# Kernel tuning notes

Measured on AMD Instinct MI355X. Metric: run time of the kernel, lower is better.

Reference implementation:

```python
import jax, jax.numpy as jnp
import numpy as np

DIM = 768      # embedding dim
NH = 12        # num heads
HD = DIM // NH # head dim = 64
WS = 7         # window size
BASE = 100.0   # rope base
TAU = 0.01     # cosine attention temperature


def _rope_tables(Wn):
    # 2D RoPE: first half of head_dim rotates with row index, second half with col index.
    quarter = HD // 4
    inv = BASE ** (-2.0 * jnp.arange(quarter, dtype=jnp.float32) / (HD // 2))  # [HD/4]
    yy, xx = jnp.meshgrid(jnp.arange(Wn, dtype=jnp.float32),
                          jnp.arange(Wn, dtype=jnp.float32), indexing='ij')
    ang = jnp.concatenate([yy.reshape(-1, 1) * inv, xx.reshape(-1, 1) * inv], axis=-1)  # [W^2, HD/2]
    return jnp.sin(ang), jnp.cos(ang)


def _apply_rope(t, sin, cos):
    # t: [Bw, L, nH, HD]; rotate-half within each spatial-axis block
    h = HD // 2
    t1, t2 = t[..., :h], t[..., h:]
    s = sin[None, :, None, :]
    c = cos[None, :, None, :]
    return jnp.concatenate([t1 * c - t2 * s, t1 * s + t2 * c], axis=-1)


def setup_inputs() -> dict:
    key = jax.random.key(0)
    k1, k2, k3 = jax.random.split(key, 3)
    B, H, W_img = 2, 224, 224
    x = jax.random.normal(k1, (B, H * W_img, DIM), jnp.float32)
    qkv_w = jax.random.normal(k2, (3 * DIM, DIM), jnp.float32) * 0.02
    proj_w = jax.random.normal(k3, (DIM, DIM), jnp.float32) * 0.02
    return {"x": x, "qkv_w": qkv_w, "proj_w": proj_w, "H": H, "W_img": W_img, "shift": 1}


def reference(x, qkv_w, proj_w, H, W_img, shift):
    B, N, D = x.shape
    Wn = WS
    x2d = x.reshape(B, H, W_img, D)
    ss = Wn // 2 if shift else 0
    if shift:
        x2d = jnp.roll(x2d, (-ss, -ss), axis=(1, 2))
    pad_b = (-H) % Wn
    pad_r = (-W_img) % Wn
    if pad_b or pad_r:
        x2d = jnp.pad(x2d, ((0, 0), (0, pad_b), (0, pad_r), (0, 0)))
    Hp, Wp = H + pad_b, W_img + pad_r
    # window partition: [B, Hp, Wp, D] -> [B*nW, W^2, D]
    xw = x2d.reshape(B, Hp // Wn, Wn, Wp // Wn, Wn, D).transpose(0, 1, 3, 2, 4, 5).reshape(-1, Wn * Wn, D)
    Bw, L = xw.shape[0], Wn * Wn
    qkv = xw @ qkv_w.T                       # [Bw, L, 3D]
    q, k, v = jnp.split(qkv, 3, axis=-1)
    q = q.reshape(Bw, L, NH, HD)
    k = k.reshape(Bw, L, NH, HD)
    v = v.reshape(Bw, L, NH, HD)
    sin, cos = _rope_tables(Wn)
    q = _apply_rope(q, sin, cos)
    k = _apply_rope(k, sin, cos)
    # cosine attention: L2-normalize q,k then scale by 1/tau
    q = q / jnp.clip(jnp.linalg.norm(q, axis=-1, keepdims=True), 1e-12)
    k = k / jnp.clip(jnp.linalg.norm(k, axis=-1, keepdims=True), 1e-12)
    q = q.transpose(0, 2, 1, 3)  # [Bw, nH, L, HD]
    k = k.transpose(0, 2, 1, 3)
    v = v.transpose(0, 2, 1, 3)
    attn = jax.nn.softmax(jnp.einsum('bhqd,bhkd->bhqk', q, k) / TAU, axis=-1)
    out = jnp.einsum('bhqk,bhkd->bhqd', attn, v)
    out = out.transpose(0, 2, 1, 3).reshape(Bw, L, D)
    # window reverse
    out = out.reshape(B, Hp // Wn, Wp // Wn, Wn, Wn, D).transpose(0, 1, 3, 2, 4, 5).reshape(B, Hp, Wp, D)
    out = out[:, :H, :W_img, :]
    if shift:
        out = jnp.roll(out, (ss, ss), axis=(1, 2))
    return out.reshape(B, N, D) @ proj_w.T
```

## Files before the change

### kernel.cpp

```cpp
#include <hip/hip_runtime.h>
#include <cstdint>
#include <cstddef>

typedef __bf16 bf16x8 __attribute__((ext_vector_type(8)));
typedef float  f32x4  __attribute__((ext_vector_type(4)));

typedef __attribute__((address_space(1))) void v_as1;
typedef __attribute__((address_space(3))) void v_as3;

#define NTOK 100352
#define DIMC 768
#define NHEAD 12
#define IMG 224
#define WN 7
#define WL 49

__device__ __forceinline__ unsigned short f2bf(float f) {
    uint32_t u = __float_as_uint(f);
    uint32_t r = (u + 0x7FFFu + ((u >> 16) & 1u)) >> 16;
    return (unsigned short)r;
}
__device__ __forceinline__ float bf2f(unsigned short u) {
    return __uint_as_float(((uint32_t)u) << 16);
}

__device__ __forceinline__ void async_cp16(const void* g, void* l) {
    __builtin_amdgcn_global_load_lds((v_as1*)g, (v_as3*)l, 16, 0, 0);
}

__global__ __launch_bounds__(256) void hilo_kernel(const float* __restrict__ in,
        unsigned short* __restrict__ hi, unsigned short* __restrict__ lo,
        int n4, int has_lo) {
    int idx = blockIdx.x * 256 + threadIdx.x;
    int stride = gridDim.x * 256;
    for (int i = idx; i < n4; i += stride) {
        float4 v = reinterpret_cast<const float4*>(in)[i];
        ushort4 h;
        h.x = f2bf(v.x); h.y = f2bf(v.y); h.z = f2bf(v.z); h.w = f2bf(v.w);
        reinterpret_cast<ushort4*>(hi)[i] = h;
        if (has_lo) {
            ushort4 l;
            l.x = f2bf(v.x - bf2f(h.x));
            l.y = f2bf(v.y - bf2f(h.y));
            l.z = f2bf(v.z - bf2f(h.z));
            l.w = f2bf(v.w - bf2f(h.w));
            reinterpret_cast<ushort4*>(lo)[i] = l;
        }
    }
}

#define BM 128
#define BN 128
#define BK 32
template <int TRIPLE>
__global__ __launch_bounds__(256) void gemm_bt(
    const unsigned short* __restrict__ Ahi, const unsigned short* __restrict__ Alo,
    const unsigned short* __restrict__ Bhi, const unsigned short* __restrict__ Blo,
    float* __restrict__ Cf, unsigned short* __restrict__ Cb,
    int M, int N, int K)
{
    __shared__ unsigned short lAh[BM * BK];
    __shared__ unsigned short lBh[BN * BK];
    __shared__ unsigned short lAl[BM * BK];
    __shared__ unsigned short lBl[BN * BK];

    const int tid  = threadIdx.x;
    const int wave = tid >> 6;
    const int lane = tid & 63;

    const int nTiles = N / BN;
    const int bm = blockIdx.x / nTiles;
    const int bn = blockIdx.x % nTiles;
    const int m0 = bm * BM, n0 = bn * BN;

    const int wm = (wave & 1) * 64;
    const int wn = (wave >> 1) * 64;

    f32x4 acc[4][4];
#pragma unroll
    for (int i = 0; i < 4; i++)
#pragma unroll
        for (int j = 0; j < 4; j++) acc[i][j] = (f32x4){0.f, 0.f, 0.f, 0.f};

    const int c0 = tid, c1 = tid + 256;
    const int ar0 = c0 >> 2, ac0 = (c0 & 3) * 8;
    const int ar1 = c1 >> 2, ac1 = (c1 & 3) * 8;
    const size_t off0 = (size_t)(wave * 64) * 8;
    const size_t off1 = (size_t)(256 + wave * 64) * 8;

    const int lquad = lane >> 4;
    const int l16   = lane & 15;

    const unsigned short* AhB = Ahi + (size_t)m0 * K;
    const unsigned short* BhB = Bhi + (size_t)n0 * K;
    const unsigned short* AlB = TRIPLE ? Alo + (size_t)m0 * K : nullptr;
    const unsigned short* BlB = TRIPLE ? Blo + (size_t)n0 * K : nullptr;

    for (int kk = 0; kk < K; kk += BK) {
        async_cp16(AhB + (size_t)ar0 * K + kk + ac0, &lAh[off0]);
        async_cp16(AhB + (size_t)ar1 * K + kk + ac1, &lAh[off1]);
        async_cp16(BhB + (size_t)ar0 * K + kk + ac0, &lBh[off0]);
        async_cp16(BhB + (size_t)ar1 * K + kk + ac1, &lBh[off1]);
        if (TRIPLE) {
            async_cp16(AlB + (size_t)ar0 * K + kk + ac0, &lAl[off0]);
            async_cp16(AlB + (size_t)ar1 * K + kk + ac1, &lAl[off1]);
            async_cp16(BlB + (size_t)ar0 * K + kk + ac0, &lBl[off0]);
            async_cp16(BlB + (size_t)ar1 * K + kk + ac1, &lBl[off1]);
        }
        __syncthreads();
        bf16x8 ah[4], bh[4];
#pragma unroll
        for (int i = 0; i < 4; i++)
            ah[i] = *reinterpret_cast<const bf16x8*>(&lAh[(size_t)(wm + i * 16 + l16) * BK + lquad * 8]);
#pragma unroll
        for (int j = 0; j < 4; j++)
            bh[j] = *reinterpret_cast<const bf16x8*>(&lBh[(size_t)(wn + j * 16 + l16) * BK + lquad * 8]);
#pragma unroll
        for (int i = 0; i < 4; i++)
#pragma unroll
            for (int j = 0; j < 4; j++)
                acc[i][j] = __builtin_amdgcn_mfma_f32_16x16x32_bf16(ah[i], bh[j], acc[i][j], 0, 0, 0);
        if (TRIPLE) {
            bf16x8 al[4], bl[4];
#pragma unroll
            for (int i = 0; i < 4; i++)
                al[i] = *reinterpret_cast<const bf16x8*>(&lAl[(size_t)(wm + i * 16 + l16) * BK + lquad * 8]);
#pragma unroll
            for (int j = 0; j < 4; j++)
                bl[j] = *reinterpret_cast<const bf16x8*>(&lBl[(size_t)(wn + j * 16 + l16) * BK + lquad * 8]);
#pragma unroll
            for (int i = 0; i < 4; i++)
#pragma unroll
                for (int j = 0; j < 4; j++) {
                    acc[i][j] = __builtin_amdgcn_mfma_f32_16x16x32_bf16(al[i], bh[j], acc[i][j], 0, 0, 0);
                    acc[i][j] = __builtin_amdgcn_mfma_f32_16x16x32_bf16(ah[i], bl[j], acc[i][j], 0, 0, 0);
                }
        }
        __syncthreads();
    }

    if (Cf) {
#pragma unroll
        for (int i = 0; i < 4; i++) {
            int rb = m0 + wm + i * 16 + lquad * 4;
#pragma unroll
            for (int r = 0; r < 4; r++) {
                float* crow = Cf + (size_t)(rb + r) * N + n0 + wn + l16;
#pragma unroll
                for (int j = 0; j < 4; j++) crow[j * 16] = acc[i][j][r];
            }
        }
    } else {
#pragma unroll
        for (int i = 0; i < 4; i++) {
            int rb = m0 + wm + i * 16 + lquad * 4;
#pragma unroll
            for (int r = 0; r < 4; r++) {
                unsigned short* crow = Cb + (size_t)(rb + r) * N + n0 + wn + l16;
#pragma unroll
                for (int j = 0; j < 4; j++) crow[j * 16] = f2bf(acc[i][j][r]);
            }
        }
    }
}

__global__ __launch_bounds__(256) void attn_kernel(
    const float* __restrict__ qk,
    const unsigned short* __restrict__ vbuf,
    unsigned short* __restrict__ attnout)
{
    const int h   = blockIdx.x % NHEAD;
    const int win = blockIdx.x / NHEAD;
    const int b   = win >> 10;
    const int wy  = (win >> 5) & 31;
    const int wx  = win & 31;

    __shared__ __align__(16) float sq[52][68];
    __shared__ __align__(16) float sk[52][68];
    __shared__ __align__(16) unsigned short sv[52][68];
    __shared__ __align__(16) float sS[52][52];
    __shared__ float rsum[WL];
    __shared__ int   rowidx[WL];

    const int tid = threadIdx.x;

    if (tid < WL) {
        int i = tid / WN, j = tid % WN;
        int ys = (wy * WN + i + 3) % IMG;
        int xs = (wx * WN + j + 3) % IMG;
        rowidx[tid] = b * (IMG * IMG) + ys * IMG + xs;
    }
    __syncthreads();

    const float LOG2_100_D16 = 0.41524101186092f;
    {
        const int hw = tid >> 5;
        const int t  = tid & 31;
        for (int pass = 0; pass < 7; ++pass) {
            int l = pass * 8 + hw;
            if (l < 49) {
                int i = l / WN, j = l % WN;
                float pos = (t < 16) ? (float)i : (float)j;
                float ang = pos * exp2f(-(float)(t & 15) * LOG2_100_D16);
                float s, c;
                __sincosf(ang, &s, &c);
                size_t base = (size_t)rowidx[l] * 1536 + h * 64;
                float q1 = qk[base + t], q2 = qk[base + t + 32];
                float k1 = qk[base + 768 + t], k2 = qk[base + 768 + t + 32];
                float nq = q1 * q1 + q2 * q2;
                float nk = k1 * k1 + k2 * k2;
#pragma unroll
                for (int m = 1; m < 32; m <<= 1) {
                    nq += __shfl_xor(nq, m);
                    nk += __shfl_xor(nk, m);
                }
                float iq = 10.f / fmaxf(sqrtf(nq), 1e-12f);
                float ik = 10.f / fmaxf(sqrtf(nk), 1e-12f);
                sq[l][t]      = (q1 * c - q2 * s) * iq;
                sq[l][t + 32] = (q1 * s + q2 * c) * iq;
                sk[l][t]      = (k1 * c - k2 * s) * ik;
                sk[l][t + 32] = (k1 * s + k2 * c) * ik;
            } else if (l < 52) {
                sq[l][t] = 0.f; sq[l][t + 32] = 0.f;
                sk[l][t] = 0.f; sk[l][t + 32] = 0.f;
            }
        }
    }
    for (int e = tid; e < 52 * 64; e += 256) {
        int l = e >> 6, d = e & 63;
        sv[l][d] = (l < 49) ? vbuf[(size_t)rowidx[l] * 768 + h * 64 + d] : (unsigned short)0;
    }
    __syncthreads();

    if (tid < 169) {
        int ta = tid / 13, tb = tid - ta * 13;
        int a0 = ta * 4, b0 = tb * 4;
        float acc[4][4];
#pragma unroll
        for (int i = 0; i < 4; i++)
#pragma unroll
            for (int j = 0; j < 4; j++) acc[i][j] = 0.f;
#pragma unroll 4
        for (int d4 = 0; d4 < 16; ++d4) {
            float4 qa[4], kb[4];
#pragma unroll
            for (int i = 0; i < 4; i++) qa[i] = *reinterpret_cast<const float4*>(&sq[a0 + i][d4 * 4]);
#pragma unroll
            for (int j = 0; j < 4; j++) kb[j] = *reinterpret_cast<const float4*>(&sk[b0 + j][d4 * 4]);
#pragma unroll
            for (int i = 0; i < 4; i++)
#pragma unroll
                for (int j = 0; j < 4; j++)
                    acc[i][j] += qa[i].x * kb[j].x + qa[i].y * kb[j].y +
                                 qa[i].z * kb[j].z + qa[i].w * kb[j].w;
        }
#pragma unroll
        for (int i = 0; i < 4; i++) {
            float4 r;
            r.x = (b0 + 0 < WL) ? acc[i][0] : -1e30f;
            r.y = (b0 + 1 < WL) ? acc[i][1] : -1e30f;
            r.z = (b0 + 2 < WL) ? acc[i][2] : -1e30f;
            r.w = (b0 + 3 < WL) ? acc[i][3] : -1e30f;
            *reinterpret_cast<float4*>(&sS[a0 + i][b0]) = r;
        }
    }
    __syncthreads();

    if (tid < WL * 4) {
        int a = tid >> 2, s4 = tid & 3;
        float m = -1e30f;
        for (int bb = s4; bb < WL; bb += 4) m = fmaxf(m, sS[a][bb]);
        m = fmaxf(m, __shfl_xor(m, 1));
        m = fmaxf(m, __shfl_xor(m, 2));
        float sum = 0.f;
        for (int bb = s4; bb < WL; bb += 4) {
            float p = __expf(sS[a][bb] - m);
            sS[a][bb] = p;
            sum += p;
        }
        sum += __shfl_xor(sum, 1);
        sum += __shfl_xor(sum, 2);
        if (s4 == 0) rsum[a] = 1.f / sum;
    }
    __syncthreads();

    if (tid < 208) {
        int ta = tid >> 4, td = tid & 15;
        int a0 = ta * 4, d0 = td * 4;
        float acc[4][4];
#pragma unroll
        for (int i = 0; i < 4; i++)
#pragma unroll
            for (int j = 0; j < 4; j++) acc[i][j] = 0.f;
        for (int bb = 0; bb < WL; ++bb) {
            float p0 = sS[a0 + 0][bb], p1 = sS[a0 + 1][bb];
            float p2 = sS[a0 + 2][bb], p3 = sS[a0 + 3][bb];
            ushort4 vr = *reinterpret_cast<const ushort4*>(&sv[bb][d0]);
            float v0 = bf2f(vr.x), v1 = bf2f(vr.y), v2 = bf2f(vr.z), v3 = bf2f(vr.w);
            acc[0][0] += p0 * v0; acc[0][1] += p0 * v1; acc[0][2] += p0 * v2; acc[0][3] += p0 * v3;
            acc[1][0] += p1 * v0; acc[1][1] += p1 * v1; acc[1][2] += p1 * v2; acc[1][3] += p1 * v3;
            acc[2][0] += p2 * v0; acc[2][1] += p2 * v1; acc[2][2] += p2 * v2; acc[2][3] += p2 * v3;
            acc[3][0] += p3 * v0; acc[3][1] += p3 * v1; acc[3][2] += p3 * v2; acc[3][3] += p3 * v3;
        }
#pragma unroll
        for (int i = 0; i < 4; i++) {
            int a = a0 + i;
            if (a < WL) {
                float r = rsum[a];
                ushort4 o;
                o.x = f2bf(acc[i][0] * r);
                o.y = f2bf(acc[i][1] * r);
                o.z = f2bf(acc[i][2] * r);
                o.w = f2bf(acc[i][3] * r);
                *reinterpret_cast<ushort4*>(&attnout[(size_t)rowidx[a] * 768 + h * 64 + d0]) = o;
            }
        }
    }
}

extern "C" void kernel_launch(void* const* d_in, const int* in_sizes, int n_in,
                              void* d_out, int out_size, void* d_ws, size_t ws_size,
                              hipStream_t stream) {
    const float* x      = (const float*)d_in[0];
    const float* qkv_w  = (const float*)d_in[1];
    const float* proj_w = (const float*)d_in[2];
    float* out = (float*)d_out;

    char* ws = (char*)d_ws;
    const size_t XE    = (size_t)NTOK * DIMC;
    const size_t WQKV  = (size_t)3 * DIMC * DIMC;
    const size_t WPROJ = (size_t)DIMC * DIMC;

    unsigned short* x_hi = (unsigned short*)ws;
    unsigned short* x_lo = x_hi + XE;
    unsigned short* w_hi = x_lo + XE;
    unsigned short* w_lo = w_hi + WQKV;
    unsigned short* p_hi = w_lo + WQKV;
    float* qkbuf = (float*)(p_hi + WPROJ);
    unsigned short* vbuf    = x_lo;
    unsigned short* attnout = x_hi;

    size_t need = (size_t)((char*)(qkbuf + (size_t)NTOK * 1536) - ws);
    if (ws_size < need) return;

    hilo_kernel<<<8192, 256, 0, stream>>>(x, x_hi, x_lo, (int)(XE / 4), 1);
    hilo_kernel<<<1728, 256, 0, stream>>>(qkv_w, w_hi, w_lo, (int)(WQKV / 4), 1);
    hilo_kernel<<<576, 256, 0, stream>>>(proj_w, p_hi, (unsigned short*)nullptr, (int)(WPROJ / 4), 0);

    gemm_bt<1><<<(NTOK / 128) * (1536 / 128), 256, 0, stream>>>(
        x_hi, x_lo, w_hi, w_lo, qkbuf, (unsigned short*)nullptr, NTOK, 1536, DIMC);
    gemm_bt<0><<<(NTOK / 128) * (768 / 128), 256, 0, stream>>>(
        x_hi, (unsigned short*)nullptr, w_hi + (size_t)1536 * DIMC, (unsigned short*)nullptr,
        (float*)nullptr, vbuf, NTOK, 768, DIMC);

    attn_kernel<<<2048 * NHEAD, 256, 0, stream>>>(qkbuf, vbuf, attnout);

    gemm_bt<0><<<(NTOK / 128) * (768 / 128), 256, 0, stream>>>(
        attnout, (unsigned short*)nullptr, p_hi, (unsigned short*)nullptr,
        out, (unsigned short*)nullptr, NTOK, 768, DIMC);
}
```

Baseline: 2.487 ms.

## Add 256x256 pipelined split-bf16 GEMM kernel for QK projection

Replaces the 128x128 templated GEMM for the QK projection with a dedicated 512-thread kernel using 256x256 tiles. It double-buffers hi and lo LDS staging with async copies interleaved between MFMA groups, raises wave priority around the MFMA blocks, and remaps workgroup IDs across 8 groups for cache locality. The aim is more operand reuse per LDS load and overlap of global loads with the three-MFMA compensated product. In exchange it uses much more LDS and registers, which lowers occupancy, and relies on hand-tuned waitcnt and barrier ordering.

```diff
diff --git a/kernel.cpp b/kernel.cpp
--- a/kernel.cpp
+++ b/kernel.cpp
@@ -164,6 +164,141 @@
     }
 }
 
+#define QBM 256
+#define QBN 256
+#define QBK 32
+
+__global__ __launch_bounds__(512) void gemm_qk(
+    const unsigned short* __restrict__ Ahi, const unsigned short* __restrict__ Alo,
+    const unsigned short* __restrict__ Bhi, const unsigned short* __restrict__ Blo,
+    float* __restrict__ C, int M, int N, int K)
+{
+    __shared__ __align__(16) unsigned short lA[2][2][QBM * QBK];
+    __shared__ __align__(16) unsigned short lB[2][2][QBN * QBK];
+
+    const int tid  = threadIdx.x;
+    const int wave = tid >> 6;
+    const int lane = tid & 63;
+    const int l16  = lane & 15;
+    const int lq   = lane >> 4;
+
+    const int nwg = gridDim.x;
+    const int cpx = nwg >> 3;
+    const int bid = blockIdx.x;
+    const int wg  = (bid & 7) * cpx + (bid >> 3);
+
+    const int nTiles = N / QBN;
+    const int bm = wg / nTiles, bn = wg % nTiles;
+    const int m0 = bm * QBM, n0 = bn * QBN;
+
+    const int wm = (wave >> 2) * 128;
+    const int wn = (wave & 3) * 64;
+
+    const unsigned short* Ah = Ahi + (size_t)m0 * K;
+    const unsigned short* Al = Alo + (size_t)m0 * K;
+    const unsigned short* Bh = Bhi + (size_t)n0 * K;
+    const unsigned short* Bl = Blo + (size_t)n0 * K;
+
+    const size_t goff0 = (size_t)(tid >> 2) * K + (size_t)(tid & 3) * 8;
+    const size_t goff1 = goff0 + (size_t)128 * K;
+    const int s0e = wave * 512;
+    const int s1e = 4096 + wave * 512;
+
+    const int NT = K / QBK;
+
+    f32x4 acc[8][4];
+#pragma unroll
+    for (int i = 0; i < 8; i++)
+#pragma unroll
+        for (int j = 0; j < 4; j++) acc[i][j] = (f32x4){0.f, 0.f, 0.f, 0.f};
+
+#define STG(dst, gb, kk) do { \
+        async_cp16((gb) + goff0 + (size_t)(kk), &(dst)[s0e]); \
+        async_cp16((gb) + goff1 + (size_t)(kk), &(dst)[s1e]); } while (0)
+
+#define PBAR do { asm volatile("" ::: "memory"); \
+        __builtin_amdgcn_s_barrier(); \
+        asm volatile("" ::: "memory"); } while (0)
+
+#define LGW0 do { asm volatile("s_waitcnt lgkmcnt(0)" ::: "memory"); \
+        __builtin_amdgcn_sched_barrier(0); } while (0)
+
+#define MF(H, G) do { \
+    _Pragma("unroll") for (int ii = 0; ii < 4; ++ii) { \
+      _Pragma("unroll") for (int jj = 0; jj < 2; ++jj) { \
+        const int j = (G) * 2 + jj; \
+        f32x4 a = acc[(H) * 4 + ii][j]; \
+        a = __builtin_amdgcn_mfma_f32_16x16x32_bf16(ah[ii], bh[j], a, 0, 0, 0); \
+        a = __builtin_amdgcn_mfma_f32_16x16x32_bf16(al[ii], bh[j], a, 0, 0, 0); \
+        a = __builtin_amdgcn_mfma_f32_16x16x32_bf16(ah[ii], bl[j], a, 0, 0, 0); \
+        acc[(H) * 4 + ii][j] = a; } } } while (0)
+
+    STG(lA[0][0], Ah, 0); STG(lA[0][1], Al, 0);
+    STG(lB[0][0], Bh, 0); STG(lB[0][1], Bl, 0);
+    STG(lB[1][1], Bl, QBK);
+    asm volatile("s_waitcnt vmcnt(2)" ::: "memory");
+    PBAR;
+
+#define TILE(T, CUR, NXT) do { \
+    bf16x8 ah[4], al[4], bh[4], bl[4]; \
+     \
+    _Pragma("unroll") for (int j = 0; j < 4; ++j) { \
+        bh[j] = *reinterpret_cast<const bf16x8*>(&lB[CUR][0][(wn + j * 16 + l16) * QBK + lq * 8]); \
+        bl[j] = *reinterpret_cast<const bf16x8*>(&lB[CUR][1][(wn + j * 16 + l16) * QBK + lq * 8]); } \
+    _Pragma("unroll") for (int ii = 0; ii < 4; ++ii) { \
+        ah[ii] = *reinterpret_cast<const bf16x8*>(&lA[CUR][0][(wm + ii * 16 + l16) * QBK + lq * 8]); \
+        al[ii] = *reinterpret_cast<const bf16x8*>(&lA[CUR][1][(wm + ii * 16 + l16) * QBK + lq * 8]); } \
+    if ((T) + 1 < NT) STG(lA[NXT][0], Ah, ((T) + 1) * QBK); \
+    PBAR; LGW0; \
+    __builtin_amdgcn_s_setprio(1); MF(0, 0); __builtin_amdgcn_s_setprio(0); \
+    PBAR; \
+     \
+    if ((T) + 1 < NT) STG(lA[NXT][1], Al, ((T) + 1) * QBK); \
+    PBAR; \
+    __builtin_amdgcn_s_setprio(1); MF(0, 1); __builtin_amdgcn_s_setprio(0); \
+    PBAR; \
+     \
+    _Pragma("unroll") for (int ii = 0; ii < 4; ++ii) { \
+        ah[ii] = *reinterpret_cast<const bf16x8*>(&lA[CUR][0][(wm + 64 + ii * 16 + l16) * QBK + lq * 8]); \
+        al[ii] = *reinterpret_cast<const bf16x8*>(&lA[CUR][1][(wm + 64 + ii * 16 + l16) * QBK + lq * 8]); } \
+    if ((T) + 1 < NT) STG(lB[NXT][0], Bh, ((T) + 1) * QBK); \
+    PBAR; LGW0; \
+    __builtin_amdgcn_s_setprio(1); MF(1, 1); __builtin_amdgcn_s_setprio(0); \
+    PBAR; \
+     \
+    if ((T) + 2 < NT) STG(lB[CUR][1], Bl, ((T) + 2) * QBK); \
+    PBAR; \
+    __builtin_amdgcn_s_setprio(1); MF(1, 0); __builtin_amdgcn_s_setprio(0); \
+    if ((T) + 1 < NT) { \
+        if ((T) + 2 < NT) { asm volatile("s_waitcnt vmcnt(2)" ::: "memory"); } \
+        else              { asm volatile("s_waitcnt vmcnt(0)" ::: "memory"); } \
+    } \
+    PBAR; \
+} while (0)
+
+    for (int t = 0; t < NT; t += 2) {
+        TILE(t, 0, 1);
+        TILE(t + 1, 1, 0);
+    }
+
+#undef TILE
+#undef MF
+#undef LGW0
+#undef PBAR
+#undef STG
+
+#pragma unroll
+    for (int i = 0; i < 8; ++i) {
+        const int rb = m0 + wm + i * 16 + lq * 4;
+#pragma unroll
+        for (int r = 0; r < 4; ++r) {
+            float* crow = C + (size_t)(rb + r) * N + n0 + wn + l16;
+#pragma unroll
+            for (int j = 0; j < 4; ++j) crow[j * 16] = acc[i][j][r];
+        }
+    }
+}
+
 __global__ __launch_bounds__(256) void attn_kernel(
     const float* __restrict__ qk,
     const unsigned short* __restrict__ vbuf,
@@ -347,8 +482,8 @@
     hilo_kernel<<<1728, 256, 0, stream>>>(qkv_w, w_hi, w_lo, (int)(WQKV / 4), 1);
     hilo_kernel<<<576, 256, 0, stream>>>(proj_w, p_hi, (unsigned short*)nullptr, (int)(WPROJ / 4), 0);
 
-    gemm_bt<1><<<(NTOK / 128) * (1536 / 128), 256, 0, stream>>>(
-        x_hi, x_lo, w_hi, w_lo, qkbuf, (unsigned short*)nullptr, NTOK, 1536, DIMC);
+    gemm_qk<<<(NTOK / 256) * (1536 / 256), 512, 0, stream>>>(
+        x_hi, x_lo, w_hi, w_lo, qkbuf, NTOK, 1536, DIMC);
     gemm_bt<0><<<(NTOK / 128) * (768 / 128), 256, 0, stream>>>(
         x_hi, (unsigned short*)nullptr, w_hi + (size_t)1536 * DIMC, (unsigned short*)nullptr,
         (float*)nullptr, vbuf, NTOK, 768, DIMC);
```

Measured after the change: 2.322 ms. 6.6% less time.
